# Kernel optimization log

Hardware: AMD Instinct MI355X
Metric: run time of the kernel (lower is better)

Reference implementation:

```python
import jax, jax.numpy as jnp
import numpy as np

N_EXPERTS = 64
TOP_K = 8
NORM_TOPK = True
SCALING = 1.0


def setup_inputs() -> dict:
    key = jax.random.key(0)
    logits = jax.random.normal(key, (524288, N_EXPERTS), dtype=jnp.float32)
    return {"logits": logits}


def reference(logits):
    # scoring_func == 'softmax': softmax over expert dim in float32
    routing_weights = jax.nn.softmax(logits.astype(jnp.float32), axis=1)
    # top-k experts per token: values and indices, sorted descending (matches torch.topk)
    topk_weights, topk_ids = jax.lax.top_k(routing_weights, TOP_K)  # [T, K]
    if NORM_TOPK:
        topk_weights = topk_weights / jnp.sum(topk_weights, axis=-1, keepdims=True)
    if SCALING != 1.0:
        topk_weights = topk_weights * SCALING
    # torch.histc(topk_ids, bins=E, min=0, max=E) == bincount over flat ids (float output)
    tokens_per_expert = jnp.zeros((N_EXPERTS,), dtype=jnp.float32).at[topk_ids.ravel()].add(1.0)
    return (logits, routing_weights, topk_weights, topk_ids, tokens_per_expert)
```

## Files before the change

### kernel.cpp

```cpp
#include <hip/hip_runtime.h>
#include <math.h>

#define NEXP 64
#define TOPK 8
#define TILE 128
#define PITCH 65

typedef float v4 __attribute__((ext_vector_type(4)));

__device__ __forceinline__ void stage_tile(const v4* __restrict__ buf,
                                           v4* __restrict__ gpass,
                                           float* __restrict__ tile,
                                           int w, int l)
{
    #pragma unroll
    for (int k = 0; k < 16; ++k) {
        int i = (w << 10) + l + (k << 6);
        v4 v = buf[k];
        __builtin_nontemporal_store(v, &gpass[i]);
        int r  = i >> 4;
        int c4 = (i & 15) << 2;
        float* b = &tile[r * PITCH + c4];
        b[0] = v.x; b[1] = v.y; b[2] = v.z; b[3] = v.w;
    }
}

__device__ __forceinline__ void load_tile(v4* __restrict__ buf,
                                          const v4* __restrict__ g, int l)
{
    #pragma unroll
    for (int k = 0; k < 16; ++k)
        buf[k] = __builtin_nontemporal_load(&g[l + (k << 6)]);
}

__device__ __forceinline__ void compute_tile(const float* __restrict__ tile,
                                             const v4* __restrict__ buf,
                                             float* __restrict__ out_rw,
                                             float* __restrict__ out_tw,
                                             float* __restrict__ out_ti,
                                             float* shist,
                                             long tokBase, int w, int l, int tid)
{
    const float* __restrict__ row = &tile[tid * PITCH];
    float vals[TOPK], ids[TOPK];
    #pragma unroll
    for (int j = 0; j < TOPK; ++j) { vals[j] = -INFINITY; ids[j] = 0.0f; }
    float ssum = 0.0f;

    #pragma unroll 8
    for (int e = 0; e < NEXP; ++e) {
        float x = row[e];
        ssum += __expf(x);
        float fe = (float)e;
        bool c[TOPK];
        #pragma unroll
        for (int j = 0; j < TOPK; ++j) c[j] = x > vals[j];
        #pragma unroll
        for (int j = TOPK - 1; j >= 1; --j) {
            ids[j]  = c[j] ? (c[j - 1] ? ids[j - 1] : fe) : ids[j];
            vals[j] = __builtin_amdgcn_fmed3f(x, vals[j - 1], vals[j]);
        }
        ids[0]  = c[0] ? fe : ids[0];
        vals[0] = fmaxf(vals[0], x);
    }
    const float sinv = 1.0f / ssum;

    float ew[TOPK];
    float tsum = 0.0f;
    #pragma unroll
    for (int j = 0; j < TOPK; ++j) { ew[j] = __expf(vals[j]); tsum += ew[j]; }
    const float tinv = 1.0f / tsum;

    const long tok = tokBase + tid;
    v4* twp = (v4*)out_tw + tok * 2;
    v4* tip = (v4*)out_ti + tok * 2;
    v4 w0 = { ew[0] * tinv, ew[1] * tinv, ew[2] * tinv, ew[3] * tinv };
    v4 w1 = { ew[4] * tinv, ew[5] * tinv, ew[6] * tinv, ew[7] * tinv };
    v4 i0 = { ids[0], ids[1], ids[2], ids[3] };
    v4 i1 = { ids[4], ids[5], ids[6], ids[7] };
    __builtin_nontemporal_store(w0, &twp[0]);
    __builtin_nontemporal_store(w1, &twp[1]);
    __builtin_nontemporal_store(i0, &tip[0]);
    __builtin_nontemporal_store(i1, &tip[1]);

    #pragma unroll
    for (int j = 0; j < TOPK; ++j)
        atomicAdd(&shist[(int)ids[j]], 1.0f);

    v4* grw = (v4*)out_rw + tokBase * (NEXP / 4);
    #pragma unroll
    for (int k = 0; k < 16; ++k) {
        int i = (w << 10) + l + (k << 6);
        float si = __shfl(sinv, (l >> 4) + 4 * k);
        v4 x = buf[k];
        v4 o;
        o.x = __expf(x.x) * si;
        o.y = __expf(x.y) * si;
        o.z = __expf(x.z) * si;
        o.w = __expf(x.w) * si;
        __builtin_nontemporal_store(o, &grw[i]);
    }
}

__global__ __launch_bounds__(TILE) void router_kernel(
    const float* __restrict__ logits,
    float* __restrict__ out_logits,
    float* __restrict__ out_rw,
    float* __restrict__ out_tw,
    float* __restrict__ out_ti,
    float* __restrict__ out_hist,
    int nTiles)
{
    __shared__ float tile[TILE * PITCH];
    __shared__ float shist[NEXP];

    const int tid = threadIdx.x;
    const int w   = tid >> 6;
    const int l   = tid & 63;
    if (tid < NEXP) shist[tid] = 0.0f;
    __syncthreads();

    const int grid = gridDim.x;
    const int tA = blockIdx.x;
    const int tB = tA + grid;

    const long baseA = (long)tA * TILE;
    v4 bufA[16], bufB[16];

    load_tile(bufA, (const v4*)logits + baseA * (NEXP / 4), (w << 10) / 64 ? l : l);
    {
        const v4* gA = (const v4*)logits + baseA * (NEXP / 4) + (w << 10);
        #pragma unroll
        for (int k = 0; k < 16; ++k)
            bufA[k] = __builtin_nontemporal_load(&gA[l + (k << 6)]);
    }
    stage_tile(bufA, (v4*)out_logits + baseA * (NEXP / 4), tile, w, l);

    const bool hasB = tB < nTiles;
    const long baseB = (long)tB * TILE;
    if (hasB) {
        const v4* gB = (const v4*)logits + baseB * (NEXP / 4) + (w << 10);
        #pragma unroll
        for (int k = 0; k < 16; ++k)
            bufB[k] = __builtin_nontemporal_load(&gB[l + (k << 6)]);
    }

    compute_tile(tile, bufA, out_rw, out_tw, out_ti, shist, baseA, w, l, tid);

    if (hasB) {
        stage_tile(bufB, (v4*)out_logits + baseB * (NEXP / 4), tile, w, l);
        compute_tile(tile, bufB, out_rw, out_tw, out_ti, shist, baseB, w, l, tid);
    }

    __syncthreads();
    if (tid < NEXP) atomicAdd(&out_hist[tid], shist[tid]);
}

extern "C" void kernel_launch(void* const* d_in, const int* in_sizes, int n_in,
                              void* d_out, int out_size, void* d_ws, size_t ws_size,
                              hipStream_t stream) {
    const float* logits = (const float*)d_in[0];
    const long T = (long)in_sizes[0] / NEXP;

    float* out      = (float*)d_out;
    float* o_logits = out;
    float* o_rw     = out + T * NEXP;
    float* o_tw     = out + 2 * T * NEXP;
    float* o_ti     = o_tw + T * TOPK;
    float* o_hist   = o_ti + T * TOPK;

    (void)hipMemsetAsync(o_hist, 0, NEXP * sizeof(float), stream);

    const int nTiles = (int)(T / TILE);
    const int grid   = (nTiles + 1) / 2;
    router_kernel<<<grid, TILE, 0, stream>>>(logits, o_logits, o_rw, o_tw, o_ti,
                                             o_hist, nTiles);
}
```

Baseline: 109.0 us.

## Use persistent grid with rolling prefetch and move histogram to separate kernel

The router kernel becomes a grid-stride persistent loop capped at 1024 blocks. It alternates two register buffers so the next tile's logits load is issued while the current tile is computed. The per-token shared-memory histogram atomics are removed from the hot kernel, and a second kernel rebuilds the histogram by re-reading the top-k id output. This trades fewer resident blocks and an extra launch plus an extra read of the id array for better load/compute overlap and a lighter main kernel.

```diff
diff --git a/kernel.cpp b/kernel.cpp
--- a/kernel.cpp
+++ b/kernel.cpp
@@ -5,14 +5,26 @@
 #define TOPK 8
 #define TILE 128
 #define PITCH 65
+#define MAXGRID 1024
 
 typedef float v4 __attribute__((ext_vector_type(4)));
 
+__device__ __forceinline__ void load_wave(v4* __restrict__ buf,
+                                          const float* __restrict__ logits,
+                                          long tokBase, int w, int l)
+{
+    const v4* g = (const v4*)logits + tokBase * (NEXP / 4) + (w << 10);
+    #pragma unroll
+    for (int k = 0; k < 16; ++k)
+        buf[k] = __builtin_nontemporal_load(&g[l + (k << 6)]);
+}
+
 __device__ __forceinline__ void stage_tile(const v4* __restrict__ buf,
-                                           v4* __restrict__ gpass,
+                                           float* __restrict__ out_logits,
                                            float* __restrict__ tile,
-                                           int w, int l)
+                                           long tokBase, int w, int l)
 {
+    v4* gpass = (v4*)out_logits + tokBase * (NEXP / 4);
     #pragma unroll
     for (int k = 0; k < 16; ++k) {
         int i = (w << 10) + l + (k << 6);
@@ -25,20 +37,11 @@
     }
 }
 
-__device__ __forceinline__ void load_tile(v4* __restrict__ buf,
-                                          const v4* __restrict__ g, int l)
-{
-    #pragma unroll
-    for (int k = 0; k < 16; ++k)
-        buf[k] = __builtin_nontemporal_load(&g[l + (k << 6)]);
-}
-
 __device__ __forceinline__ void compute_tile(const float* __restrict__ tile,
                                              const v4* __restrict__ buf,
                                              float* __restrict__ out_rw,
                                              float* __restrict__ out_tw,
                                              float* __restrict__ out_ti,
-                                             float* shist,
                                              long tokBase, int w, int l, int tid)
 {
     const float* __restrict__ row = &tile[tid * PITCH];
@@ -83,10 +86,6 @@
     __builtin_nontemporal_store(i0, &tip[0]);
     __builtin_nontemporal_store(i1, &tip[1]);
 
-    #pragma unroll
-    for (int j = 0; j < TOPK; ++j)
-        atomicAdd(&shist[(int)ids[j]], 1.0f);
-
     v4* grw = (v4*)out_rw + tokBase * (NEXP / 4);
     #pragma unroll
     for (int k = 0; k < 16; ++k) {
@@ -108,50 +107,52 @@
     float* __restrict__ out_rw,
     float* __restrict__ out_tw,
     float* __restrict__ out_ti,
-    float* __restrict__ out_hist,
     int nTiles)
 {
     __shared__ float tile[TILE * PITCH];
-    __shared__ float shist[NEXP];
-
     const int tid = threadIdx.x;
     const int w   = tid >> 6;
     const int l   = tid & 63;
+    const int stride = gridDim.x;
+
+    v4 bufA[16], bufB[16];
+    int tb = blockIdx.x;
+    load_wave(bufA, logits, (long)tb * TILE, w, l);
+
+    for (; tb < nTiles; tb += 2 * stride) {
+        const long baseA = (long)tb * TILE;
+        stage_tile(bufA, out_logits, tile, baseA, w, l);
+        const int t1 = tb + stride;
+        if (t1 < nTiles) load_wave(bufB, logits, (long)t1 * TILE, w, l);
+        compute_tile(tile, bufA, out_rw, out_tw, out_ti, baseA, w, l, tid);
+
+        if (t1 < nTiles) {
+            const long baseB = (long)t1 * TILE;
+            stage_tile(bufB, out_logits, tile, baseB, w, l);
+            const int t2 = tb + 2 * stride;
+            if (t2 < nTiles) load_wave(bufA, logits, (long)t2 * TILE, w, l);
+            compute_tile(tile, bufB, out_rw, out_tw, out_ti, baseB, w, l, tid);
+        }
+    }
+}
+
+__global__ __launch_bounds__(256) void hist_kernel(
+    const float* __restrict__ ti, float* __restrict__ out_hist, int n4)
+{
+    __shared__ float shist[NEXP];
+    const int tid = threadIdx.x;
     if (tid < NEXP) shist[tid] = 0.0f;
     __syncthreads();
 
-    const int grid = gridDim.x;
-    const int tA = blockIdx.x;
-    const int tB = tA + grid;
-
-    const long baseA = (long)tA * TILE;
-    v4 bufA[16], bufB[16];
-
-    load_tile(bufA, (const v4*)logits + baseA * (NEXP / 4), (w << 10) / 64 ? l : l);
-    {
-        const v4* gA = (const v4*)logits + baseA * (NEXP / 4) + (w << 10);
-        #pragma unroll
-        for (int k = 0; k < 16; ++k)
-            bufA[k] = __builtin_nontemporal_load(&gA[l + (k << 6)]);
+    const v4* t4 = (const v4*)ti;
+    const int step = gridDim.x * 256;
+    for (int i = blockIdx.x * 256 + tid; i < n4; i += step) {
+        v4 v = t4[i];
+        atomicAdd(&shist[(int)v.x], 1.0f);
+        atomicAdd(&shist[(int)v.y], 1.0f);
+        atomicAdd(&shist[(int)v.z], 1.0f);
+        atomicAdd(&shist[(int)v.w], 1.0f);
     }
-    stage_tile(bufA, (v4*)out_logits + baseA * (NEXP / 4), tile, w, l);
-
-    const bool hasB = tB < nTiles;
-    const long baseB = (long)tB * TILE;
-    if (hasB) {
-        const v4* gB = (const v4*)logits + baseB * (NEXP / 4) + (w << 10);
-        #pragma unroll
-        for (int k = 0; k < 16; ++k)
-            bufB[k] = __builtin_nontemporal_load(&gB[l + (k << 6)]);
-    }
-
-    compute_tile(tile, bufA, out_rw, out_tw, out_ti, shist, baseA, w, l, tid);
-
-    if (hasB) {
-        stage_tile(bufB, (v4*)out_logits + baseB * (NEXP / 4), tile, w, l);
-        compute_tile(tile, bufB, out_rw, out_tw, out_ti, shist, baseB, w, l, tid);
-    }
-
     __syncthreads();
     if (tid < NEXP) atomicAdd(&out_hist[tid], shist[tid]);
 }
@@ -172,7 +173,10 @@
     (void)hipMemsetAsync(o_hist, 0, NEXP * sizeof(float), stream);
 
     const int nTiles = (int)(T / TILE);
-    const int grid   = (nTiles + 1) / 2;
+    const int grid   = nTiles < MAXGRID ? nTiles : MAXGRID;
     router_kernel<<<grid, TILE, 0, stream>>>(logits, o_logits, o_rw, o_tw, o_ti,
-                                             o_hist, nTiles);
+                                             nTiles);
+
+    const int n4 = (int)(T * TOPK / 4);
+    hist_kernel<<<256, 256, 0, stream>>>(o_ti, o_hist, n4);
 }
```

New measurement: 124.7 us. 1.14x slower.
